# Kernel optimization log

Hardware: AMD Instinct MI355X
Metric: run time of the kernel (lower is better)

Reference implementation:

```python
import jax, jax.numpy as jnp
import numpy as np

N_NODES = 100000
N_EDGES = 1600000
D_IN = 128
D_H = 128
NUM_GRAPHS = 128


def setup_inputs() -> dict:
    key = jax.random.key(0)
    ks = jax.random.split(key, 16)
    x = jax.random.normal(ks[0], (N_NODES, D_IN), dtype=jnp.float32)
    edge_index = jax.random.randint(ks[1], (2, N_EDGES), 0, N_NODES, dtype=jnp.int64)
    batch_index = jnp.sort(jax.random.randint(ks[2], (N_NODES,), 0, NUM_GRAPHS, dtype=jnp.int64))
    s = 0.05
    W1 = s * jax.random.normal(ks[3], (D_IN, D_H), dtype=jnp.float32)
    b1 = jnp.zeros((D_H,), jnp.float32)
    W2 = s * jax.random.normal(ks[4], (D_H, D_H), dtype=jnp.float32)
    b2 = jnp.zeros((D_H,), jnp.float32)
    W3 = s * jax.random.normal(ks[5], (D_H, D_H), dtype=jnp.float32)
    b3 = jnp.zeros((D_H,), jnp.float32)
    W4 = s * jax.random.normal(ks[6], (D_H, D_H), dtype=jnp.float32)
    b4 = jnp.zeros((D_H,), jnp.float32)
    Wl = s * jax.random.normal(ks[7], (2 * D_H, 1), dtype=jnp.float32)
    bl = jnp.zeros((1,), jnp.float32)
    return {"x": x, "edge_index": edge_index, "batch_index": batch_index,
            "W1": W1, "b1": b1, "W2": W2, "b2": b2, "W3": W3, "b3": b3,
            "W4": W4, "b4": b4, "Wl": Wl, "bl": bl}


def _gcn_prep(edge_index, n_nodes):
    # add self-loops, symmetric normalization D^-1/2 (A+I) D^-1/2
    loops = jnp.arange(n_nodes, dtype=edge_index.dtype)
    row = jnp.concatenate([edge_index[0], loops])  # source
    col = jnp.concatenate([edge_index[1], loops])  # target
    deg = jax.ops.segment_sum(jnp.ones_like(col, dtype=jnp.float32), col,
                              num_segments=n_nodes)
    dinv = jnp.where(deg > 0, jax.lax.rsqrt(jnp.maximum(deg, 1.0)), 0.0)
    norm = dinv[row] * dinv[col]  # [E+N]
    return row, col, norm


def _gcn(h, W, b, row, col, norm, n_nodes):
    h = h @ W                                   # [N, H]
    msg = h[row] * norm[:, None]                # gather + scale
    return jax.ops.segment_sum(msg, col, num_segments=n_nodes) + b


def reference(x, edge_index, batch_index, W1, b1, W2, b2, W3, b3, W4, b4, Wl, bl):
    n = x.shape[0]
    row, col, norm = _gcn_prep(edge_index, n)
    h = jnp.tanh(_gcn(x, W1, b1, row, col, norm, n))
    h = jnp.tanh(_gcn(h, W2, b2, row, col, norm, n))
    h = jnp.tanh(_gcn(h, W3, b3, row, col, norm, n))
    h = jnp.tanh(_gcn(h, W4, b4, row, col, norm, n))
    # global max / mean pool per graph
    cnt = jax.ops.segment_sum(jnp.ones((n,), jnp.float32), batch_index,
                              num_segments=NUM_GRAPHS)
    mx = jax.ops.segment_max(h, batch_index, num_segments=NUM_GRAPHS)
    mx = jnp.where(cnt[:, None] > 0, mx, 0.0)
    sm = jax.ops.segment_sum(h, batch_index, num_segments=NUM_GRAPHS)
    mn = sm / jnp.maximum(cnt, 1.0)[:, None]
    pooled = jnp.concatenate([mx, mn], axis=1)  # [G, 2H]
    return pooled @ Wl + bl                     # [G, 1]
```

## Files before the change

### kernel.cpp

```cpp
#include <hip/hip_runtime.h>
#include <hip/hip_bf16.h>
#include <math.h>

#define PSPLIT 8
#define BSH 5
#define BW 32
#define AST 40

typedef float v4f __attribute__((ext_vector_type(4)));
typedef float v2f __attribute__((ext_vector_type(2)));
typedef unsigned int v4u __attribute__((ext_vector_type(4)));
typedef unsigned int v2u __attribute__((ext_vector_type(2)));
typedef __attribute__((ext_vector_type(8))) short bf8;
typedef __attribute__((ext_vector_type(4))) float f4;
typedef unsigned short u16;
typedef unsigned int u32;

static inline size_t align_up(size_t x, size_t a){ return (x + a - 1) & ~(a - 1); }

__device__ inline void bf_split(float v, u16& hi, u16& lo){
  __hip_bfloat16 h = __float2bfloat16(v);
  float hf = __bfloat162float(h);
  __hip_bfloat16 l = __float2bfloat16(v - hf);
  hi = *(u16*)&h; lo = *(u16*)&l;
}

__device__ inline void fmixlo(float& a, u32 p){
  asm("v_fma_mix_f32 %0, %1, 1.0, %0 op_sel:[0,0,0] op_sel_hi:[1,0,0]" : "+v"(a) : "v"(p));
}
__device__ inline void fmixhi(float& a, u32 p){
  asm("v_fma_mix_f32 %0, %1, 1.0, %0 op_sel:[1,0,0] op_sel_hi:[1,0,0]" : "+v"(a) : "v"(p));
}

__device__ inline float tanh_fast(float x){
  float u = __builtin_amdgcn_exp2f(x * 2.8853900817779268f);
  float q = __builtin_amdgcn_rcpf(u + 1.0f);
  return fmaf(-2.0f, q, 1.0f);
}


__global__ __launch_bounds__(256) void k_bhist(const int* __restrict__ col, int* __restrict__ bcnt,
                                               int E, int NB,
                                               const int* __restrict__ batch, int* __restrict__ gstart,
                                               int n, int G){
  extern __shared__ int lh[];
  for (int i = threadIdx.x; i < NB; i += 256) lh[i] = 0;
  __syncthreads();
  for (int e = blockIdx.x * 256 + threadIdx.x; e < E; e += gridDim.x * 256)
    atomicAdd(&lh[col[e] >> BSH], 1);
  __syncthreads();
  for (int i = threadIdx.x; i < NB; i += 256){
    int v = lh[i];
    if (v) atomicAdd(&bcnt[i], v);
  }
  for (int i = blockIdx.x * 256 + threadIdx.x; i < n; i += gridDim.x * 256){
    int cb = batch[i];
    if (i == 0){ for (int g = 0; g <= cb; ++g) gstart[g] = 0; }
    else { int pb = batch[i - 1]; for (int g = pb + 1; g <= cb; ++g) gstart[g] = i; }
    if (i == n - 1){ for (int g = cb + 1; g <= G; ++g) gstart[g] = n; }
  }
}

__global__ void k_bscan(const int* __restrict__ bcnt, int* __restrict__ boff, int NB, int E,
                        int* __restrict__ rp, int N){
  __shared__ int sd[256];
  int t = threadIdx.x;
  int c[16]; int s = 0;
  const int PT = (NB + 255) / 256;
  for (int j = 0; j < PT; ++j){ int i = t * PT + j; c[j] = (i < NB) ? bcnt[i] : 0; s += c[j]; }
  sd[t] = s; __syncthreads();
  for (int off = 1; off < 256; off <<= 1){
    int v = sd[t];
    if (t >= off) v += sd[t - off];
    __syncthreads(); sd[t] = v; __syncthreads();
  }
  int run = sd[t] - s;
  for (int j = 0; j < PT; ++j){ int i = t * PT + j; if (i < NB) boff[i] = run; run += c[j]; }
  if (t == 255){ boff[NB] = run; rp[N] = E; }
}

__global__ __launch_bounds__(256) void k_bscat(const int* __restrict__ ei, const int* __restrict__ boff,
                                               int* __restrict__ bfill, unsigned* __restrict__ tmp, int E){
  int e = blockIdx.x * 256 + threadIdx.x;
  if (e >= E) return;
  int s = ei[e], d = ei[E + e];
  int b = d >> BSH;
  int p = atomicAdd(&bfill[b * 32], 1);
  tmp[boff[b] + p] = (unsigned)s | ((unsigned)(d & (BW - 1)) << 17);
}

__global__ __launch_bounds__(256) void k_bfin(const unsigned* __restrict__ tmp, const int* __restrict__ boff,
                                              int* __restrict__ ssrc, int* __restrict__ rp,
                                              float* __restrict__ dinv, int N){
  int b = blockIdx.x;
  int d0 = b << BSH;
  int lim = N - d0; if (lim > BW) lim = BW;
  __shared__ int dcnt[BW], dst_[BW], lfill[BW];
  int t = threadIdx.x;
  if (t < BW){ dcnt[t] = 0; lfill[t] = 0; }
  __syncthreads();
  int lo = boff[b], hi = boff[b + 1];
  for (int i = lo + t; i < hi; i += 256) atomicAdd(&dcnt[tmp[i] >> 17], 1);
  __syncthreads();
  if (t == 0){ int run = 0; for (int l = 0; l < BW; ++l){ dst_[l] = run; run += dcnt[l]; } }
  __syncthreads();
  if (t < lim){
    int d = d0 + t;
    rp[d] = lo + dst_[t];
    double dd = (double)(dcnt[t] + 1);
    dinv[d] = (float)(1.0 / sqrt(dd));
  }
  __syncthreads();
  for (int i = lo + t; i < hi; i += 256){
    unsigned r = tmp[i];
    int l = r >> 17;
    int pos = dst_[l] + atomicAdd(&lfill[l], 1);
    ssrc[lo + pos] = (int)(r & 0x1FFFFu);
  }
}


__global__ __launch_bounds__(256) void k_cvtw(const float* __restrict__ w0, const float* __restrict__ w1,
                                              const float* __restrict__ w2, const float* __restrict__ w3,
                                              u16* __restrict__ wth, u16* __restrict__ wtl){
  int id = blockIdx.x * 256 + threadIdx.x;
  if (id >= 4 * 16384) return;
  int l = id >> 14, rem = id & 16383, k = rem >> 7, nn = rem & 127;
  const float* Wsrc = (l == 0) ? w0 : (l == 1) ? w1 : (l == 2) ? w2 : w3;
  float v = Wsrc[k * 128 + nn];
  u16 hi, lo; bf_split(v, hi, lo);
  wth[(l << 14) + nn * 128 + k] = hi;
  wtl[(l << 14) + nn * 128 + k] = lo;
}


__global__ __launch_bounds__(256, 4) void k_gemm(const float* __restrict__ A,
                                                 const u16* __restrict__ wth, const u16* __restrict__ wtl,
                                                 const float* __restrict__ dinv,
                                                 u16* __restrict__ C, int n, int packed){
  __shared__ u16 Ah[128 * AST], Al[128 * AST], Wh[128 * AST], Wl[128 * AST];
  int t = threadIdx.x;
  int r0 = blockIdx.x * 128;
  int wv = t >> 6, lane = t & 63;
  int q = lane >> 4, ln = lane & 15;

  int srow = t >> 1;
  int shalf = (t & 1) * 16;
  int grow = r0 + srow; if (grow > n - 1) grow = n - 1;
  const float* ga = A + (size_t)grow * 128 + shalf;
  const u16* gwh = wth + srow * 128 + shalf;
  const u16* gwl = wtl + srow * 128 + shalf;

  f4 acc[2][8];
  #pragma unroll
  for (int mt = 0; mt < 2; ++mt)
    #pragma unroll
    for (int nt = 0; nt < 8; ++nt) acc[mt][nt] = (f4)(0.f);

  for (int c = 0; c < 4; ++c){
    __syncthreads();
    {
      u16* ah = &Ah[srow * AST + shalf];
      u16* al = &Al[srow * AST + shalf];
      if (packed){
        const v4u* gp = (const v4u*)(ga + c * 32);
        #pragma unroll
        for (int i = 0; i < 4; ++i){
          v4u v = gp[i];
          ushort4 hv = {(u16)(v.x >> 16), (u16)(v.y >> 16), (u16)(v.z >> 16), (u16)(v.w >> 16)};
          ushort4 lv = {(u16)v.x, (u16)v.y, (u16)v.z, (u16)v.w};
          *(ushort4*)&ah[i * 4] = hv;
          *(ushort4*)&al[i * 4] = lv;
        }
      } else {
        const float4* gp = (const float4*)(ga + c * 32);
        #pragma unroll
        for (int i = 0; i < 4; ++i){
          float4 v = gp[i];
          u16 h0,h1,h2,h3,l0,l1,l2,l3;
          bf_split(v.x, h0, l0); bf_split(v.y, h1, l1);
          bf_split(v.z, h2, l2); bf_split(v.w, h3, l3);
          ushort4 hv = {h0,h1,h2,h3}, lv = {l0,l1,l2,l3};
          *(ushort4*)&ah[i * 4] = hv;
          *(ushort4*)&al[i * 4] = lv;
        }
      }
    }
    {
      const u16* ph = gwh + c * 32;
      const u16* pl = gwl + c * 32;
      bf8 h0 = *(const bf8*)ph, h1 = *(const bf8*)(ph + 8);
      bf8 l0 = *(const bf8*)pl, l1 = *(const bf8*)(pl + 8);
      *(bf8*)&Wh[srow * AST + shalf] = h0; *(bf8*)&Wh[srow * AST + shalf + 8] = h1;
      *(bf8*)&Wl[srow * AST + shalf] = l0; *(bf8*)&Wl[srow * AST + shalf + 8] = l1;
    }
    __syncthreads();

    bf8 afh[2], afl[2];
    #pragma unroll
    for (int mt = 0; mt < 2; ++mt){
      int row = wv * 32 + mt * 16 + ln;
      afh[mt] = *(const bf8*)&Ah[row * AST + q * 8];
      afl[mt] = *(const bf8*)&Al[row * AST + q * 8];
    }
    #pragma unroll
    for (int nt = 0; nt < 8; ++nt){
      int wn = nt * 16 + ln;
      bf8 wfh = *(const bf8*)&Wh[wn * AST + q * 8];
      bf8 wfl = *(const bf8*)&Wl[wn * AST + q * 8];
      #pragma unroll
      for (int mt = 0; mt < 2; ++mt){
        acc[mt][nt] = __builtin_amdgcn_mfma_f32_16x16x32_bf16(afh[mt], wfh, acc[mt][nt], 0, 0, 0);
        acc[mt][nt] = __builtin_amdgcn_mfma_f32_16x16x32_bf16(afl[mt], wfh, acc[mt][nt], 0, 0, 0);
        acc[mt][nt] = __builtin_amdgcn_mfma_f32_16x16x32_bf16(afh[mt], wfl, acc[mt][nt], 0, 0, 0);
      }
    }
  }

  #pragma unroll
  for (int mt = 0; mt < 2; ++mt){
    int base_m = r0 + wv * 32 + mt * 16 + q * 4;
    float dv[4];
    #pragma unroll
    for (int reg = 0; reg < 4; ++reg){
      int row = base_m + reg;
      dv[reg] = (row < n) ? dinv[row] : 0.f;
    }
    #pragma unroll
    for (int nt = 0; nt < 8; ++nt){
      #pragma unroll
      for (int reg = 0; reg < 4; ++reg){
        int row = base_m + reg;
        if (row < n){
          _Float16 hv = (_Float16)(acc[mt][nt][reg] * dv[reg]);
          C[(size_t)row * 128 + nt * 16 + ln] = *(u16*)&hv;
        }
      }
    }
  }
}


__global__ __launch_bounds__(256) void k_agg(const u16* __restrict__ hwp, const int* __restrict__ rp,
                                             const int* __restrict__ ssrc,
                                             const float* __restrict__ dinv, const float* __restrict__ bias,
                                             float* __restrict__ hout, int n, int pack){
  int node = blockIdx.x * 4 + (threadIdx.x >> 6);
  node = __builtin_amdgcn_readfirstlane(node);
  if (node >= n) return;
  int lane = threadIdx.x & 63;
  const u32* hw32 = (const u32*)hwp;

  int e0 = rp[node], e1 = rp[node + 1];
  float a0 = 0.f, a1 = 0.f;
  int e = e0;
  while (e + 16 <= e1){
    u32 p[16];
    #pragma unroll
    for (int i = 0; i < 16; ++i){
      int s = ssrc[e + i];
      p[i] = hw32[(size_t)s * 64 + lane];
    }
    #pragma unroll
    for (int i = 0; i < 16; ++i){ fmixlo(a0, p[i]); fmixhi(a1, p[i]); }
    e += 16;
  }
  while (e + 4 <= e1){
    u32 p[4];
    #pragma unroll
    for (int i = 0; i < 4; ++i){
      int s = ssrc[e + i];
      p[i] = hw32[(size_t)s * 64 + lane];
    }
    #pragma unroll
    for (int i = 0; i < 4; ++i){ fmixlo(a0, p[i]); fmixhi(a1, p[i]); }
    e += 4;
  }
  while (e < e1){
    int s = ssrc[e];
    u32 p = hw32[(size_t)s * 64 + lane];
    fmixlo(a0, p); fmixhi(a1, p);
    ++e;
  }
  {
    u32 p = hw32[(size_t)node * 64 + lane];
    fmixlo(a0, p); fmixhi(a1, p);
  }
  float di = dinv[node];
  v2f bv = *(const v2f*)(bias + lane * 2);
  float r0 = tanh_fast(fmaf(a0, di, bv.x));
  float r1 = tanh_fast(fmaf(a1, di, bv.y));
  if (pack){
    u16 h0, h1, l0, l1;
    bf_split(r0, h0, l0); bf_split(r1, h1, l1);
    v2u pv;
    pv.x = ((u32)h0 << 16) | l0;
    pv.y = ((u32)h1 << 16) | l1;
    __builtin_nontemporal_store(pv, (v2u*)((u32*)hout + (size_t)node * 128 + lane * 2));
  } else {
    v2f rr; rr.x = r0; rr.y = r1;
    __builtin_nontemporal_store(rr, (v2f*)(hout + (size_t)node * 128 + lane * 2));
  }
}


__global__ __launch_bounds__(256) void k_pool1(const float* __restrict__ h, const int* __restrict__ gstart,
                                               float* __restrict__ pmx, float* __restrict__ psm){
  int g = blockIdx.x >> 3, s = blockIdx.x & (PSPLIT - 1);
  int t = threadIdx.x;
  int fq = t & 31;
  int rw = t >> 5;
  int i0 = gstart[g], i1 = gstart[g + 1];
  int len = i1 - i0;
  int chunk = (len + PSPLIT - 1) / PSPLIT;
  int a = i0 + s * chunk;
  int b = a + chunk; if (b > i1) b = i1;

  const v4f* hv = (const v4f*)h;
  v4f mx = (v4f)(-INFINITY), sm = (v4f)(0.f);
  for (int i = a + rw; i < b; i += 8){
    v4f v = hv[(size_t)i * 32 + fq];
    mx.x = fmaxf(mx.x, v.x); mx.y = fmaxf(mx.y, v.y);
    mx.z = fmaxf(mx.z, v.z); mx.w = fmaxf(mx.w, v.w);
    sm += v;
  }
  __shared__ v4f smx[8][32], ssm[8][32];
  smx[rw][fq] = mx; ssm[rw][fq] = sm;
  __syncthreads();
  if (rw == 0){
    #pragma unroll
    for (int r2 = 1; r2 < 8; ++r2){
      v4f m2 = smx[r2][fq], s2 = ssm[r2][fq];
      mx.x = fmaxf(mx.x, m2.x); mx.y = fmaxf(mx.y, m2.y);
      mx.z = fmaxf(mx.z, m2.z); mx.w = fmaxf(mx.w, m2.w);
      sm += s2;
    }
    ((v4f*)pmx)[(size_t)blockIdx.x * 32 + fq] = mx;
    ((v4f*)psm)[(size_t)blockIdx.x * 32 + fq] = sm;
  }
}

__global__ __launch_bounds__(128) void k_head(const float* __restrict__ pmx, const float* __restrict__ psm,
                                              const int* __restrict__ gstart,
                                              const float* __restrict__ Wl, const float* __restrict__ bl,
                                              float* __restrict__ out){
  int g = blockIdx.x, f = threadIdx.x;
  float mx = -INFINITY, sm = 0.f;
  #pragma unroll
  for (int s = 0; s < PSPLIT; ++s){
    mx = fmaxf(mx, pmx[((size_t)g * PSPLIT + s) * 128 + f]);
    sm += psm[((size_t)g * PSPLIT + s) * 128 + f];
  }
  int cnt = gstart[g + 1] - gstart[g];
  if (cnt <= 0) mx = 0.f;
  float mn = sm / (float)(cnt > 0 ? cnt : 1);
  float contrib = mx * Wl[f] + mn * Wl[128 + f];
  for (int o = 32; o > 0; o >>= 1) contrib += __shfl_down(contrib, o);
  __shared__ float sred[2];
  if ((f & 63) == 0) sred[f >> 6] = contrib;
  __syncthreads();
  if (f == 0) out[g] = sred[0] + sred[1] + bl[0];
}


extern "C" void kernel_launch(void* const* d_in, const int* in_sizes, int n_in,
                              void* d_out, int out_size, void* d_ws, size_t ws_size,
                              hipStream_t stream){
  const float* x     = (const float*)d_in[0];
  const int*   ei    = (const int*)d_in[1];
  const int*   batch = (const int*)d_in[2];
  const float* W[4]  = {(const float*)d_in[3], (const float*)d_in[5], (const float*)d_in[7], (const float*)d_in[9]};
  const float* B[4]  = {(const float*)d_in[4], (const float*)d_in[6], (const float*)d_in[8], (const float*)d_in[10]};
  const float* Wl    = (const float*)d_in[11];
  const float* bl    = (const float*)d_in[12];
  float* out = (float*)d_out;

  int N = in_sizes[0] / 128;
  int E = in_sizes[1] / 2;
  int G = out_size;
  int NB = (N + BW - 1) >> BSH;

  char* ws = (char*)d_ws;
  size_t off = 0;
  auto alloc = [&](size_t bytes) -> void* {
    void* p = ws + off; off = align_up(off + bytes, 256); return p;
  };
  float* dinv  = (float*)alloc((size_t)N * 4);
  int*   rp    = (int*)  alloc((size_t)(N + 1) * 4);
  int*   bcnt  = (int*)  alloc((size_t)(NB + 1) * 4);
  int*   boff  = (int*)  alloc((size_t)(NB + 1) * 4);
  int*   bfill = (int*)  alloc((size_t)NB * 32 * 4);
  int*   gst   = (int*)  alloc((size_t)(G + 1) * 4);
  int*   ssrc  = (int*)  alloc((size_t)E * 4);
  u16*   wth   = (u16*)  alloc((size_t)4 * 16384 * 2);
  u16*   wtl   = (u16*)  alloc((size_t)4 * 16384 * 2);
  float* pmx   = (float*)alloc((size_t)G * PSPLIT * 128 * 4);
  float* psm   = (float*)alloc((size_t)G * PSPLIT * 128 * 4);
  u16*   hw    = (u16*)  alloc((size_t)N * 128 * 2);
  float* h     = (float*)alloc((size_t)N * 128 * 4);
  unsigned* tmp = (unsigned*)hw;

  hipMemsetAsync(bcnt, 0, (size_t)(NB + 1) * 4, stream);
  hipMemsetAsync(bfill, 0, (size_t)NB * 32 * 4, stream);

  int gE = (E + 255) / 256;
  k_cvtw <<<256, 256, 0, stream>>>(W[0], W[1], W[2], W[3], wth, wtl);
  k_bhist<<<128, 256, NB * 4, stream>>>(ei + E, bcnt, E, NB, batch, gst, N, G);
  k_bscan<<<1, 256, 0, stream>>>(bcnt, boff, NB, E, rp, N);
  k_bscat<<<gE, 256, 0, stream>>>(ei, boff, bfill, tmp, E);
  k_bfin <<<NB, 256, 0, stream>>>(tmp, boff, ssrc, rp, dinv, N);

  int gemmG = (N + 127) / 128;
  int aggG  = (N + 3) / 4;
  const float* hin = x;
  for (int l = 0; l < 4; ++l){
    k_gemm<<<gemmG, 256, 0, stream>>>(hin, wth + (l << 14), wtl + (l << 14), dinv, hw, N, l > 0);
    k_agg <<<aggG, 256, 0, stream>>>(hw, rp, ssrc, dinv, B[l], h, N, l < 3);
    hin = h;
  }
  k_pool1<<<G * PSPLIT, 256, 0, stream>>>(h, gst, pmx, psm);
  k_head <<<G, 128, 0, stream>>>(pmx, psm, gst, Wl, bl, out);
}
```

Before: 579.6 us.

## Split bucket scatter counters into per-edge-group sub-buckets to cut atomic contention

The edge list is partitioned into eight contiguous groups. Histogram and scatter counters become per (bucket, group), so atomics on each bucket's fill counter are spread across eight separate counters, and the scan now runs over the larger sub-bucket array. Edge index loads use nontemporal hints. The cost is a bigger scan done by a single block (NB8 is about 25k entries, so roughly 98 per thread) and larger memsets.

```diff
diff --git a/kernel.cpp b/kernel.cpp
--- a/kernel.cpp
+++ b/kernel.cpp
@@ -5,6 +5,7 @@
 #define PSPLIT 8
 #define BSH 5
 #define BW 32
+#define NGRP 8
 #define AST 40
 
 typedef float v4f __attribute__((ext_vector_type(4)));
@@ -39,35 +40,41 @@
 }
 
 
-__global__ __launch_bounds__(256) void k_bhist(const int* __restrict__ col, int* __restrict__ bcnt,
+__global__ __launch_bounds__(256) void k_bhist(const int* __restrict__ col, int* __restrict__ cnt8,
                                                int E, int NB,
                                                const int* __restrict__ batch, int* __restrict__ gstart,
                                                int n, int G){
   extern __shared__ int lh[];
   for (int i = threadIdx.x; i < NB; i += 256) lh[i] = 0;
   __syncthreads();
-  for (int e = blockIdx.x * 256 + threadIdx.x; e < E; e += gridDim.x * 256)
-    atomicAdd(&lh[col[e] >> BSH], 1);
+  int EPG = (E + NGRP - 1) / NGRP;
+  int g   = blockIdx.x >> 4;
+  int sub = blockIdx.x & 15;
+  int gbeg = g * EPG;
+  int gend = gbeg + EPG; if (gend > E) gend = E;
+  for (int e = gbeg + sub * 256 + threadIdx.x; e < gend; e += 16 * 256)
+    atomicAdd(&lh[__builtin_nontemporal_load(col + e) >> BSH], 1);
   __syncthreads();
   for (int i = threadIdx.x; i < NB; i += 256){
     int v = lh[i];
-    if (v) atomicAdd(&bcnt[i], v);
+    if (v) atomicAdd(&cnt8[i * NGRP + g], v);
   }
   for (int i = blockIdx.x * 256 + threadIdx.x; i < n; i += gridDim.x * 256){
     int cb = batch[i];
-    if (i == 0){ for (int g = 0; g <= cb; ++g) gstart[g] = 0; }
-    else { int pb = batch[i - 1]; for (int g = pb + 1; g <= cb; ++g) gstart[g] = i; }
-    if (i == n - 1){ for (int g = cb + 1; g <= G; ++g) gstart[g] = n; }
-  }
-}
-
-__global__ void k_bscan(const int* __restrict__ bcnt, int* __restrict__ boff, int NB, int E,
+    if (i == 0){ for (int gg = 0; gg <= cb; ++gg) gstart[gg] = 0; }
+    else { int pb = batch[i - 1]; for (int gg = pb + 1; gg <= cb; ++gg) gstart[gg] = i; }
+    if (i == n - 1){ for (int gg = cb + 1; gg <= G; ++gg) gstart[gg] = n; }
+  }
+}
+
+__global__ void k_bscan(const int* __restrict__ cnt8, int* __restrict__ boff8, int NB8, int E,
                         int* __restrict__ rp, int N){
   __shared__ int sd[256];
   int t = threadIdx.x;
-  int c[16]; int s = 0;
-  const int PT = (NB + 255) / 256;
-  for (int j = 0; j < PT; ++j){ int i = t * PT + j; c[j] = (i < NB) ? bcnt[i] : 0; s += c[j]; }
+  const int PT = (NB8 + 255) / 256;
+  int base = t * PT;
+  int s = 0;
+  for (int j = 0; j < PT; ++j){ int i = base + j; if (i < NB8) s += cnt8[i]; }
   sd[t] = s; __syncthreads();
   for (int off = 1; off < 256; off <<= 1){
     int v = sd[t];
@@ -75,21 +82,31 @@
     __syncthreads(); sd[t] = v; __syncthreads();
   }
   int run = sd[t] - s;
-  for (int j = 0; j < PT; ++j){ int i = t * PT + j; if (i < NB) boff[i] = run; run += c[j]; }
-  if (t == 255){ boff[NB] = run; rp[N] = E; }
-}
-
-__global__ __launch_bounds__(256) void k_bscat(const int* __restrict__ ei, const int* __restrict__ boff,
-                                               int* __restrict__ bfill, unsigned* __restrict__ tmp, int E){
-  int e = blockIdx.x * 256 + threadIdx.x;
-  if (e >= E) return;
-  int s = ei[e], d = ei[E + e];
-  int b = d >> BSH;
-  int p = atomicAdd(&bfill[b * 32], 1);
-  tmp[boff[b] + p] = (unsigned)s | ((unsigned)(d & (BW - 1)) << 17);
-}
-
-__global__ __launch_bounds__(256) void k_bfin(const unsigned* __restrict__ tmp, const int* __restrict__ boff,
+  for (int j = 0; j < PT; ++j){
+    int i = base + j;
+    if (i < NB8){ boff8[i] = run; run += cnt8[i]; }
+  }
+  if (t == 255){ boff8[NB8] = run; rp[N] = E; }
+}
+
+__global__ __launch_bounds__(256) void k_bscat(const int* __restrict__ ei, const int* __restrict__ boff8,
+                                               int* __restrict__ bfill8, unsigned* __restrict__ tmp, int E){
+  int g   = blockIdx.x >> 8;
+  int bpg = blockIdx.x & 255;
+  int EPG = (E + NGRP - 1) / NGRP;
+  int gbeg = g * EPG;
+  int gend = gbeg + EPG; if (gend > E) gend = E;
+  for (int e = gbeg + bpg * 256 + threadIdx.x; e < gend; e += 256 * 256){
+    int d = __builtin_nontemporal_load(ei + E + e);
+    int s = __builtin_nontemporal_load(ei + e);
+    int b = d >> BSH;
+    int idx = b * NGRP + g;
+    int p = atomicAdd(&bfill8[idx * 16], 1);
+    tmp[boff8[idx] + p] = (unsigned)s | ((unsigned)(d & (BW - 1)) << 17);
+  }
+}
+
+__global__ __launch_bounds__(256) void k_bfin(const unsigned* __restrict__ tmp, const int* __restrict__ boff8,
                                               int* __restrict__ ssrc, int* __restrict__ rp,
                                               float* __restrict__ dinv, int N){
   int b = blockIdx.x;
@@ -99,7 +116,7 @@
   int t = threadIdx.x;
   if (t < BW){ dcnt[t] = 0; lfill[t] = 0; }
   __syncthreads();
-  int lo = boff[b], hi = boff[b + 1];
+  int lo = boff8[b * NGRP], hi = boff8[(b + 1) * NGRP];
   for (int i = lo + t; i < hi; i += 256) atomicAdd(&dcnt[tmp[i] >> 17], 1);
   __syncthreads();
   if (t == 0){ int run = 0; for (int l = 0; l < BW; ++l){ dst_[l] = run; run += dcnt[l]; } }
@@ -379,6 +396,7 @@
   int E = in_sizes[1] / 2;
   int G = out_size;
   int NB = (N + BW - 1) >> BSH;
+  int NB8 = NB * NGRP;
 
   char* ws = (char*)d_ws;
   size_t off = 0;
@@ -387,9 +405,9 @@
   };
   float* dinv  = (float*)alloc((size_t)N * 4);
   int*   rp    = (int*)  alloc((size_t)(N + 1) * 4);
-  int*   bcnt  = (int*)  alloc((size_t)(NB + 1) * 4);
-  int*   boff  = (int*)  alloc((size_t)(NB + 1) * 4);
-  int*   bfill = (int*)  alloc((size_t)NB * 32 * 4);
+  int*   cnt8  = (int*)  alloc((size_t)(NB8 + 1) * 4);
+  int*   boff8 = (int*)  alloc((size_t)(NB8 + 1) * 4);
+  int*   bfill8= (int*)  alloc((size_t)NB8 * 16 * 4);
   int*   gst   = (int*)  alloc((size_t)(G + 1) * 4);
   int*   ssrc  = (int*)  alloc((size_t)E * 4);
   u16*   wth   = (u16*)  alloc((size_t)4 * 16384 * 2);
@@ -400,15 +418,14 @@
   float* h     = (float*)alloc((size_t)N * 128 * 4);
   unsigned* tmp = (unsigned*)hw;
 
-  hipMemsetAsync(bcnt, 0, (size_t)(NB + 1) * 4, stream);
-  hipMemsetAsync(bfill, 0, (size_t)NB * 32 * 4, stream);
-
-  int gE = (E + 255) / 256;
+  hipMemsetAsync(cnt8, 0, (size_t)(NB8 + 1) * 4, stream);
+  hipMemsetAsync(bfill8, 0, (size_t)NB8 * 16 * 4, stream);
+
   k_cvtw <<<256, 256, 0, stream>>>(W[0], W[1], W[2], W[3], wth, wtl);
-  k_bhist<<<128, 256, NB * 4, stream>>>(ei + E, bcnt, E, NB, batch, gst, N, G);
-  k_bscan<<<1, 256, 0, stream>>>(bcnt, boff, NB, E, rp, N);
-  k_bscat<<<gE, 256, 0, stream>>>(ei, boff, bfill, tmp, E);
-  k_bfin <<<NB, 256, 0, stream>>>(tmp, boff, ssrc, rp, dinv, N);
+  k_bhist<<<128, 256, NB * 4, stream>>>(ei + E, cnt8, E, NB, batch, gst, N, G);
+  k_bscan<<<1, 256, 0, stream>>>(cnt8, boff8, NB8, E, rp, N);
+  k_bscat<<<NGRP * 256, 256, 0, stream>>>(ei, boff8, bfill8, tmp, E);
+  k_bfin <<<NB, 256, 0, stream>>>(tmp, boff8, ssrc, rp, dinv, N);
 
   int gemmG = (N + 127) / 128;
   int aggG  = (N + 3) / 4;
```

Result: slower. 650.8 us (+12.3%).

## Bucket edges by 256-node ranges with block-local staged scatter in LDS

Applied to the files above, without the earlier changes.

Destination buckets widen from 32 to 256 nodes (NB about 391), and the edge scatter kernel now processes 8192-edge chunks per block. Each chunk builds a local histogram in shared memory, reserves one global range per bucket with a single atomic, stages the edges in LDS, and writes them out contiguously. The aim is to replace one global atomic per edge with one per bucket per block and to make the writes to tmp coalesced. The finalize kernel now uses a 256-wide parallel scan for per-node offsets. This assumes NB never exceeds 512, and the larger buckets mean fewer, heavier blocks in the finalize kernel.

```diff
diff --git a/kernel.cpp b/kernel.cpp
--- a/kernel.cpp
+++ b/kernel.cpp
@@ -3,8 +3,9 @@
 #include <math.h>
 
 #define PSPLIT 8
-#define BSH 5
-#define BW 32
+#define BSH 8
+#define NBMAX 512
+#define CHUNK 8192
 #define AST 40
 
 typedef float v4f __attribute__((ext_vector_type(4)));
@@ -80,13 +81,58 @@
 }
 
 __global__ __launch_bounds__(256) void k_bscat(const int* __restrict__ ei, const int* __restrict__ boff,
-                                               int* __restrict__ bfill, unsigned* __restrict__ tmp, int E){
-  int e = blockIdx.x * 256 + threadIdx.x;
-  if (e >= E) return;
-  int s = ei[e], d = ei[E + e];
-  int b = d >> BSH;
-  int p = atomicAdd(&bfill[b * 32], 1);
-  tmp[boff[b] + p] = (unsigned)s | ((unsigned)(d & (BW - 1)) << 17);
+                                               int* __restrict__ bfill, unsigned* __restrict__ tmp,
+                                               int E, int NB){
+  __shared__ int lh[NBMAX], loff[NBMAX], gb[NBMAX], lfil[NBMAX];
+  __shared__ int sd[256];
+  __shared__ int sumA;
+  __shared__ u32 stg[CHUNK];
+  int t = threadIdx.x;
+  const int* col = ei + E;
+  int c0 = blockIdx.x * CHUNK;
+  int c1 = c0 + CHUNK; if (c1 > E) c1 = E;
+
+  for (int i = t; i < NBMAX; i += 256){ lh[i] = 0; lfil[i] = 0; }
+  __syncthreads();
+  for (int e = c0 + t; e < c1; e += 256)
+    atomicAdd(&lh[col[e] >> BSH], 1);
+  __syncthreads();
+  sd[t] = lh[t]; __syncthreads();
+  for (int off = 1; off < 256; off <<= 1){
+    int v = sd[t];
+    if (t >= off) v += sd[t - off];
+    __syncthreads(); sd[t] = v; __syncthreads();
+  }
+  loff[t] = sd[t] - lh[t];
+  if (t == 255) sumA = sd[255];
+  __syncthreads();
+  int lb = lh[256 + t];
+  sd[t] = lb; __syncthreads();
+  for (int off = 1; off < 256; off <<= 1){
+    int v = sd[t];
+    if (t >= off) v += sd[t - off];
+    __syncthreads(); sd[t] = v; __syncthreads();
+  }
+  loff[256 + t] = sumA + sd[t] - lb;
+  for (int i = t; i < NB; i += 256){
+    int c = lh[i];
+    gb[i] = c ? (boff[i] + atomicAdd(&bfill[i * 16], c)) : 0;
+  }
+  __syncthreads();
+  for (int e = c0 + t; e < c1; e += 256){
+    int d = col[e], s = ei[e];
+    int b = d >> BSH;
+    int p = atomicAdd(&lfil[b], 1);
+    stg[loff[b] + p] = (unsigned)s | ((unsigned)(d & 255) << 17);
+  }
+  __syncthreads();
+  int wv = t >> 6, lane = t & 63;
+  for (int b = wv; b < NB; b += 4){
+    int len = lh[b];
+    if (!len) continue;
+    int base = gb[b], lo = loff[b];
+    for (int j = lane; j < len; j += 64) tmp[base + j] = stg[lo + j];
+  }
 }
 
 __global__ __launch_bounds__(256) void k_bfin(const unsigned* __restrict__ tmp, const int* __restrict__ boff,
@@ -94,27 +140,35 @@
                                               float* __restrict__ dinv, int N){
   int b = blockIdx.x;
   int d0 = b << BSH;
-  int lim = N - d0; if (lim > BW) lim = BW;
-  __shared__ int dcnt[BW], dst_[BW], lfill[BW];
+  int lim = N - d0; if (lim > 256) lim = 256;
+  __shared__ int dcnt[256], dexc[256], lfill[256];
   int t = threadIdx.x;
-  if (t < BW){ dcnt[t] = 0; lfill[t] = 0; }
+  dcnt[t] = 0; lfill[t] = 0;
   __syncthreads();
   int lo = boff[b], hi = boff[b + 1];
   for (int i = lo + t; i < hi; i += 256) atomicAdd(&dcnt[tmp[i] >> 17], 1);
   __syncthreads();
-  if (t == 0){ int run = 0; for (int l = 0; l < BW; ++l){ dst_[l] = run; run += dcnt[l]; } }
-  __syncthreads();
+  int cme = dcnt[t];
+  dexc[t] = cme; __syncthreads();
+  for (int off = 1; off < 256; off <<= 1){
+    int v = dexc[t];
+    if (t >= off) v += dexc[t - off];
+    __syncthreads(); dexc[t] = v; __syncthreads();
+  }
+  int excl = dexc[t] - cme;
+  __syncthreads();
+  dexc[t] = excl;
   if (t < lim){
     int d = d0 + t;
-    rp[d] = lo + dst_[t];
-    double dd = (double)(dcnt[t] + 1);
+    rp[d] = lo + excl;
+    double dd = (double)(cme + 1);
     dinv[d] = (float)(1.0 / sqrt(dd));
   }
   __syncthreads();
   for (int i = lo + t; i < hi; i += 256){
     unsigned r = tmp[i];
     int l = r >> 17;
-    int pos = dst_[l] + atomicAdd(&lfill[l], 1);
+    int pos = dexc[l] + atomicAdd(&lfill[l], 1);
     ssrc[lo + pos] = (int)(r & 0x1FFFFu);
   }
 }
@@ -378,7 +432,7 @@
   int N = in_sizes[0] / 128;
   int E = in_sizes[1] / 2;
   int G = out_size;
-  int NB = (N + BW - 1) >> BSH;
+  int NB = (N + 255) >> BSH;
 
   char* ws = (char*)d_ws;
   size_t off = 0;
@@ -389,7 +443,7 @@
   int*   rp    = (int*)  alloc((size_t)(N + 1) * 4);
   int*   bcnt  = (int*)  alloc((size_t)(NB + 1) * 4);
   int*   boff  = (int*)  alloc((size_t)(NB + 1) * 4);
-  int*   bfill = (int*)  alloc((size_t)NB * 32 * 4);
+  int*   bfill = (int*)  alloc((size_t)NB * 16 * 4);
   int*   gst   = (int*)  alloc((size_t)(G + 1) * 4);
   int*   ssrc  = (int*)  alloc((size_t)E * 4);
   u16*   wth   = (u16*)  alloc((size_t)4 * 16384 * 2);
@@ -401,13 +455,12 @@
   unsigned* tmp = (unsigned*)hw;
 
   hipMemsetAsync(bcnt, 0, (size_t)(NB + 1) * 4, stream);
-  hipMemsetAsync(bfill, 0, (size_t)NB * 32 * 4, stream);
-
-  int gE = (E + 255) / 256;
+  hipMemsetAsync(bfill, 0, (size_t)NB * 16 * 4, stream);
+
   k_cvtw <<<256, 256, 0, stream>>>(W[0], W[1], W[2], W[3], wth, wtl);
   k_bhist<<<128, 256, NB * 4, stream>>>(ei + E, bcnt, E, NB, batch, gst, N, G);
   k_bscan<<<1, 256, 0, stream>>>(bcnt, boff, NB, E, rp, N);
-  k_bscat<<<gE, 256, 0, stream>>>(ei, boff, bfill, tmp, E);
+  k_bscat<<<(E + CHUNK - 1) / CHUNK, 256, 0, stream>>>(ei, boff, bfill, tmp, E, NB);
   k_bfin <<<NB, 256, 0, stream>>>(tmp, boff, ssrc, rp, dinv, N);
 
   int gemmG = (N + 127) / 128;
```

Result: faster. 556.3 us (-4.0%).
